# Kernel optimization log

Hardware: AMD Instinct MI355X
Metric: run time of the kernel (lower is better)

Reference implementation:

```python
import jax, jax.numpy as jnp
import numpy as np

H = 128
NUM_IN = 384
B, N, K = 4, 2048, 48
SCALE = 30.0
EPS = 1e-5


def _layernorm(x, gamma, beta):
    mu = jnp.mean(x, axis=-1, keepdims=True)
    var = jnp.mean(jnp.square(x - mu), axis=-1, keepdims=True)
    return (x - mu) * jax.lax.rsqrt(var + EPS) * gamma + beta


def setup_inputs() -> dict:
    key = jax.random.key(0)
    ks = jax.random.split(key, 12)
    s = lambda fan_in: 1.0 / np.sqrt(fan_in)
    inp = {
        "h_V": jax.random.normal(ks[0], (B, N, H), jnp.float32),
        "h_E": jax.random.normal(ks[1], (B, N, K, NUM_IN), jnp.float32),
        "mask_V": jnp.ones((B, N), jnp.float32),
        "mask_attend": jnp.ones((B, N, K), jnp.float32),
        # message MLP
        "W1": jax.random.uniform(ks[2], (H + NUM_IN, H), jnp.float32, -s(H + NUM_IN), s(H + NUM_IN)),
        "b1": jnp.zeros((H,), jnp.float32),
        "W2": jax.random.uniform(ks[3], (H, H), jnp.float32, -s(H), s(H)),
        "b2": jnp.zeros((H,), jnp.float32),
        "W3": jax.random.uniform(ks[4], (H, H), jnp.float32, -s(H), s(H)),
        "b3": jnp.zeros((H,), jnp.float32),
        # layernorms
        "g1": jnp.ones((H,), jnp.float32), "be1": jnp.zeros((H,), jnp.float32),
        "g2": jnp.ones((H,), jnp.float32), "be2": jnp.zeros((H,), jnp.float32),
        # FFN
        "Wi": jax.random.uniform(ks[5], (H, 4 * H), jnp.float32, -s(H), s(H)),
        "bi": jnp.zeros((4 * H,), jnp.float32),
        "Wo": jax.random.uniform(ks[6], (4 * H, H), jnp.float32, -s(4 * H), s(4 * H)),
        "bo": jnp.zeros((H,), jnp.float32),
        # rezero alpha (init 0.01)
        "alpha": jnp.array([0.01], jnp.float32),
    }
    return inp


def reference(h_V, h_E, mask_V, mask_attend, W1, b1, W2, b2, W3, b3,
              g1, be1, g2, be2, Wi, bi, Wo, bo, alpha):
    gelu = lambda x: jax.nn.gelu(x, approximate=False)
    # broadcast-concat node features onto each neighbor edge: [B,N,K,H+num_in]
    h_V_expand = jnp.broadcast_to(h_V[:, :, None, :], (*h_E.shape[:-1], h_V.shape[-1]))
    h_EV = jnp.concatenate([h_V_expand, h_E], axis=-1)
    # 3-layer message MLP
    h_message = gelu(jnp.einsum("bnkf,fh->bnkh", h_EV, W1) + b1)
    h_message = gelu(jnp.einsum("bnkh,hg->bnkg", h_message, W2) + b2)
    h_message = jnp.einsum("bnkg,gh->bnkh", h_message, W3) + b3
    h_message = mask_attend[..., None] * h_message
    # masked sum-reduce over neighbors
    dh = jnp.sum(h_message, axis=-2) / SCALE
    # residual (rezero) + LayerNorm  (dropout = identity in eval)
    h = _layernorm(alpha * dh + h_V, g1, be1)
    # position-wise FFN
    dh = gelu(h @ Wi + bi) @ Wo + bo
    h = _layernorm(alpha * dh + h, g2, be2)
    # node mask
    h = mask_V[..., None] * h
    return h
```

## Files before the change

kernel.cpp:

```cpp
#include <hip/hip_runtime.h>

#define LN_EPS 1e-5f
#define RSCALE (1.0f / 30.0f)

typedef short short8  __attribute__((ext_vector_type(8)));
typedef short short4v __attribute__((ext_vector_type(4)));
typedef float f32x4   __attribute__((ext_vector_type(4)));

__device__ __forceinline__ unsigned short f2bf(float f) {
    unsigned u = __builtin_bit_cast(unsigned, f);
    u = u + 0x7FFFu + ((u >> 16) & 1u);
    return (unsigned short)(u >> 16);
}

__device__ __forceinline__ float gelu_f(float x) {
    float u  = 0.7978845608028654f * (x + 0.044715f * x * x * x);
    float e  = __expf(-2.0f * fabsf(u));
    float t  = 1.0f - 2.0f * e / (1.0f + e);
    return 0.5f * x * (1.0f + copysignf(t, u));
}

__device__ __forceinline__ f32x4 zero4() {
    f32x4 v; v.x = 0.f; v.y = 0.f; v.z = 0.f; v.w = 0.f; return v;
}

__global__ __launch_bounds__(256) void prep_w(
    const float* __restrict__ W1, const float* __restrict__ W2,
    const float* __restrict__ W3,
    unsigned short* __restrict__ w1t, unsigned short* __restrict__ w2t,
    unsigned short* __restrict__ w3t)
{
    int t = blockIdx.x * 256 + threadIdx.x;
    if (t < 65536) {
        int m = t & 127, k = t >> 7;
        w1t[m * 512 + k] = f2bf(W1[k * 128 + m]);
    } else if (t < 81920) {
        int u = t - 65536, m = u & 127, k = u >> 7;
        w2t[m * 128 + k] = f2bf(W2[k * 128 + m]);
    } else if (t < 98304) {
        int u = t - 81920, m = u & 127, k = u >> 7;
        w3t[m * 128 + k] = f2bf(W3[k * 128 + m]);
    }
}

__global__ __launch_bounds__(256, 2) void edge_mlp(
    const float* __restrict__ hV, const float* __restrict__ hE,
    const float* __restrict__ mAtt,
    const unsigned short* __restrict__ w1t, const unsigned short* __restrict__ w2t,
    const unsigned short* __restrict__ w3t,
    const float* __restrict__ b1, const float* __restrict__ b2,
    const float* __restrict__ b3, float* __restrict__ dh)
{
    __shared__ short A1[96 * 64];
    __shared__ short Wb[128 * 64];
    __shared__ short Hb[2][96 * 128];
    __shared__ float mb[96];

    const int tid  = threadIdx.x;
    const int lane = tid & 63;
    const int wv   = tid >> 6;
    const int g    = wv & 1;
    const int mh   = wv >> 1;
    const int ln   = lane & 15;
    const int kg   = lane >> 4;
    const int node0 = blockIdx.x * 2;

    if (tid < 96) mb[tid] = mAtt[node0 * 48 + tid];

    f32x4 acc[4][3];
#pragma unroll
    for (int j = 0; j < 4; ++j)
#pragma unroll
        for (int i = 0; i < 3; ++i) acc[j][i] = zero4();

    const int srow = tid >> 4;
    const int c4   = (tid & 15) * 4;
    const int kb_w = c4 >> 3;
    const int c4lo = c4 & 4;

    for (int c = 0; c < 8; ++c) {
        const int kc = c * 64;
        if (kc < 128) {
#pragma unroll
            for (int rep = 0; rep < 6; ++rep) {
                const int r = rep * 16 + srow;
                const float4 v = *(const float4*)(hV + (node0 + (r >= 48 ? 1 : 0)) * 128 + kc + c4);
                short4v p;
                p.x = (short)f2bf(v.x); p.y = (short)f2bf(v.y);
                p.z = (short)f2bf(v.z); p.w = (short)f2bf(v.w);
                *(short4v*)&A1[r * 64 + ((kb_w ^ (r & 7)) * 8) + c4lo] = p;
            }
        } else {
#pragma unroll
            for (int rep = 0; rep < 6; ++rep) {
                const int r = rep * 16 + srow;
                const float4 v = *(const float4*)(hE + (node0 * 48 + r) * 384 + (kc - 128) + c4);
                short4v p;
                p.x = (short)f2bf(v.x); p.y = (short)f2bf(v.y);
                p.z = (short)f2bf(v.z); p.w = (short)f2bf(v.w);
                *(short4v*)&A1[r * 64 + ((kb_w ^ (r & 7)) * 8) + c4lo] = p;
            }
        }
#pragma unroll
        for (int rep = 0; rep < 4; ++rep) {
            const int u = rep * 256 + tid;
            const int m = u >> 3, kb = u & 7;
            short8 val = *(const short8*)(w1t + m * 512 + kc + kb * 8);
            *(short8*)&Wb[m * 64 + ((kb ^ (m & 7)) * 8)] = val;
        }
        __syncthreads();
#pragma unroll
        for (int s = 0; s < 2; ++s) {
            const int kb = s * 4 + kg;
            short8 bf[3], af[4];
#pragma unroll
            for (int i = 0; i < 3; ++i) {
                const int r = (3 * g + i) * 16 + ln;
                bf[i] = *(const short8*)&A1[r * 64 + ((kb ^ (r & 7)) * 8)];
            }
#pragma unroll
            for (int j = 0; j < 4; ++j) {
                const int m = (4 * mh + j) * 16 + ln;
                af[j] = *(const short8*)&Wb[m * 64 + ((kb ^ (m & 7)) * 8)];
            }
#pragma unroll
            for (int j = 0; j < 4; ++j)
#pragma unroll
                for (int i = 0; i < 3; ++i)
                    acc[j][i] = __builtin_amdgcn_mfma_f32_16x16x32_bf16(af[j], bf[i], acc[j][i], 0, 0, 0);
        }
        __syncthreads();
    }

#pragma unroll
    for (int j = 0; j < 4; ++j) {
        const int m0 = (4 * mh + j) * 16 + kg * 4;
        const float4 bb = *(const float4*)(b1 + m0);
#pragma unroll
        for (int i = 0; i < 3; ++i) {
            const int r = (3 * g + i) * 16 + ln;
            short4v p;
            p.x = (short)f2bf(gelu_f(acc[j][i].x + bb.x));
            p.y = (short)f2bf(gelu_f(acc[j][i].y + bb.y));
            p.z = (short)f2bf(gelu_f(acc[j][i].z + bb.z));
            p.w = (short)f2bf(gelu_f(acc[j][i].w + bb.w));
            *(short4v*)&Hb[0][r * 128 + (((m0 >> 3) ^ (r & 7)) * 8) + (m0 & 4)] = p;
        }
    }

    for (int L = 0; L < 2; ++L) {
#pragma unroll
        for (int j = 0; j < 4; ++j)
#pragma unroll
            for (int i = 0; i < 3; ++i) acc[j][i] = zero4();

        const unsigned short* wt = (L == 0) ? w2t : w3t;
        for (int c = 0; c < 2; ++c) {
            const int kc = c * 64;
#pragma unroll
            for (int rep = 0; rep < 4; ++rep) {
                const int u = rep * 256 + tid;
                const int m = u >> 3, kb = u & 7;
                short8 val = *(const short8*)(wt + m * 128 + kc + kb * 8);
                *(short8*)&Wb[m * 64 + ((kb ^ (m & 7)) * 8)] = val;
            }
            __syncthreads();
#pragma unroll
            for (int s = 0; s < 2; ++s) {
                const int kbW = s * 4 + kg;
                const int kbH = c * 8 + s * 4 + kg;
                short8 bf[3], af[4];
#pragma unroll
                for (int i = 0; i < 3; ++i) {
                    const int r = (3 * g + i) * 16 + ln;
                    bf[i] = *(const short8*)&Hb[L][r * 128 + ((kbH ^ (r & 7)) * 8)];
                }
#pragma unroll
                for (int j = 0; j < 4; ++j) {
                    const int m = (4 * mh + j) * 16 + ln;
                    af[j] = *(const short8*)&Wb[m * 64 + ((kbW ^ (m & 7)) * 8)];
                }
#pragma unroll
                for (int j = 0; j < 4; ++j)
#pragma unroll
                    for (int i = 0; i < 3; ++i)
                        acc[j][i] = __builtin_amdgcn_mfma_f32_16x16x32_bf16(af[j], bf[i], acc[j][i], 0, 0, 0);
            }
            __syncthreads();
        }

        if (L == 0) {
#pragma unroll
            for (int j = 0; j < 4; ++j) {
                const int m0 = (4 * mh + j) * 16 + kg * 4;
                const float4 bb = *(const float4*)(b2 + m0);
#pragma unroll
                for (int i = 0; i < 3; ++i) {
                    const int r = (3 * g + i) * 16 + ln;
                    short4v p;
                    p.x = (short)f2bf(gelu_f(acc[j][i].x + bb.x));
                    p.y = (short)f2bf(gelu_f(acc[j][i].y + bb.y));
                    p.z = (short)f2bf(gelu_f(acc[j][i].z + bb.z));
                    p.w = (short)f2bf(gelu_f(acc[j][i].w + bb.w));
                    *(short4v*)&Hb[1][r * 128 + (((m0 >> 3) ^ (r & 7)) * 8) + (m0 & 4)] = p;
                }
            }
        } else {
#pragma unroll
            for (int j = 0; j < 4; ++j) {
                const int m0 = (4 * mh + j) * 16 + kg * 4;
                const float4 bb = *(const float4*)(b3 + m0);
                float s0 = 0.f, s1 = 0.f, s2 = 0.f, s3 = 0.f;
#pragma unroll
                for (int i = 0; i < 3; ++i) {
                    const int r = (3 * g + i) * 16 + ln;
                    const float mk = mb[r];
                    s0 += (acc[j][i].x + bb.x) * mk;
                    s1 += (acc[j][i].y + bb.y) * mk;
                    s2 += (acc[j][i].z + bb.z) * mk;
                    s3 += (acc[j][i].w + bb.w) * mk;
                }
#pragma unroll
                for (int off = 1; off < 16; off <<= 1) {
                    s0 += __shfl_xor(s0, off, 64);
                    s1 += __shfl_xor(s1, off, 64);
                    s2 += __shfl_xor(s2, off, 64);
                    s3 += __shfl_xor(s3, off, 64);
                }
                if (ln == 0) {
                    float4 o;
                    o.x = s0 * RSCALE; o.y = s1 * RSCALE;
                    o.z = s2 * RSCALE; o.w = s3 * RSCALE;
                    *(float4*)&dh[(node0 + g) * 128 + m0] = o;
                }
            }
        }
    }
}

__global__ __launch_bounds__(256, 2) void node_ffn(
    const float* __restrict__ hV, const float* __restrict__ dh,
    const float* __restrict__ maskV,
    const float* __restrict__ g1, const float* __restrict__ be1,
    const float* __restrict__ g2, const float* __restrict__ be2,
    const float* __restrict__ Wi, const float* __restrict__ bi,
    const float* __restrict__ Wo, const float* __restrict__ bo,
    const float* __restrict__ alphap, float* __restrict__ out)
{
    __shared__ float hbuf[16 * 132];
    __shared__ float hidb[16 * 516];
    __shared__ float obuf[16 * 132];

    const int tid = threadIdx.x;
    const float al = alphap[0];
    const int nb = blockIdx.x * 16;

    {
        const int m = tid >> 4, s = tid & 15;
        const int i0 = s * 8;
        const int base = (nb + m) * 128 + i0;
        float x[8];
        {
            float4 a0 = *(const float4*)(dh + base);
            float4 a1 = *(const float4*)(dh + base + 4);
            float4 v0 = *(const float4*)(hV + base);
            float4 v1 = *(const float4*)(hV + base + 4);
            x[0] = v0.x + al * a0.x; x[1] = v0.y + al * a0.y;
            x[2] = v0.z + al * a0.z; x[3] = v0.w + al * a0.w;
            x[4] = v1.x + al * a1.x; x[5] = v1.y + al * a1.y;
            x[6] = v1.z + al * a1.z; x[7] = v1.w + al * a1.w;
        }
        float sm = 0.f;
#pragma unroll
        for (int q = 0; q < 8; ++q) sm += x[q];
#pragma unroll
        for (int off = 1; off < 16; off <<= 1) sm += __shfl_xor(sm, off, 64);
        const float mu = sm * (1.0f / 128.0f);
        float vs = 0.f;
#pragma unroll
        for (int q = 0; q < 8; ++q) { float d = x[q] - mu; vs += d * d; }
#pragma unroll
        for (int off = 1; off < 16; off <<= 1) vs += __shfl_xor(vs, off, 64);
        const float rs = rsqrtf(vs * (1.0f / 128.0f) + LN_EPS);
#pragma unroll
        for (int q = 0; q < 8; ++q)
            hbuf[m * 132 + i0 + q] = (x[q] - mu) * rs * g1[i0 + q] + be1[i0 + q];
    }
    __syncthreads();

    {
        const int jg = tid & 127, mhh = tid >> 7;
        const int j4 = jg * 4;
        float acc[8][4];
#pragma unroll
        for (int mm = 0; mm < 8; ++mm)
#pragma unroll
            for (int jj = 0; jj < 4; ++jj) acc[mm][jj] = 0.f;
        for (int i0 = 0; i0 < 128; i0 += 4) {
            float4 w0 = *(const float4*)(Wi + (i0 + 0) * 512 + j4);
            float4 w1 = *(const float4*)(Wi + (i0 + 1) * 512 + j4);
            float4 w2 = *(const float4*)(Wi + (i0 + 2) * 512 + j4);
            float4 w3 = *(const float4*)(Wi + (i0 + 3) * 512 + j4);
#pragma unroll
            for (int mm = 0; mm < 8; ++mm) {
                float4 h4 = *(const float4*)&hbuf[(mhh * 8 + mm) * 132 + i0];
                acc[mm][0] += h4.x * w0.x + h4.y * w1.x + h4.z * w2.x + h4.w * w3.x;
                acc[mm][1] += h4.x * w0.y + h4.y * w1.y + h4.z * w2.y + h4.w * w3.y;
                acc[mm][2] += h4.x * w0.z + h4.y * w1.z + h4.z * w2.z + h4.w * w3.z;
                acc[mm][3] += h4.x * w0.w + h4.y * w1.w + h4.z * w2.w + h4.w * w3.w;
            }
        }
        float4 bb = *(const float4*)(bi + j4);
#pragma unroll
        for (int mm = 0; mm < 8; ++mm) {
            float4 o;
            o.x = gelu_f(acc[mm][0] + bb.x);
            o.y = gelu_f(acc[mm][1] + bb.y);
            o.z = gelu_f(acc[mm][2] + bb.z);
            o.w = gelu_f(acc[mm][3] + bb.w);
            *(float4*)&hidb[(mhh * 8 + mm) * 516 + j4] = o;
        }
    }
    __syncthreads();

    {
        const int m = tid >> 4;
        const int n8 = (tid & 15) * 8;
        float4 r0, r1;
        r0.x = r0.y = r0.z = r0.w = 0.f;
        r1.x = r1.y = r1.z = r1.w = 0.f;
        for (int j0 = 0; j0 < 512; j0 += 4) {
            float4 hh = *(const float4*)&hidb[m * 516 + j0];
            float hq[4] = {hh.x, hh.y, hh.z, hh.w};
#pragma unroll
            for (int jj = 0; jj < 4; ++jj) {
                float4 w0 = *(const float4*)(Wo + (j0 + jj) * 128 + n8);
                float4 w1 = *(const float4*)(Wo + (j0 + jj) * 128 + n8 + 4);
                r0.x += hq[jj] * w0.x; r0.y += hq[jj] * w0.y;
                r0.z += hq[jj] * w0.z; r0.w += hq[jj] * w0.w;
                r1.x += hq[jj] * w1.x; r1.y += hq[jj] * w1.y;
                r1.z += hq[jj] * w1.z; r1.w += hq[jj] * w1.w;
            }
        }
        float4 q0 = *(const float4*)(bo + n8);
        float4 q1 = *(const float4*)(bo + n8 + 4);
        r0.x += q0.x; r0.y += q0.y; r0.z += q0.z; r0.w += q0.w;
        r1.x += q1.x; r1.y += q1.y; r1.z += q1.z; r1.w += q1.w;
        *(float4*)&obuf[m * 132 + n8]     = r0;
        *(float4*)&obuf[m * 132 + n8 + 4] = r1;
    }
    __syncthreads();

    {
        const int m = tid >> 4, s = tid & 15;
        const int i0 = s * 8;
        float x[8];
#pragma unroll
        for (int q = 0; q < 8; ++q)
            x[q] = hbuf[m * 132 + i0 + q] + al * obuf[m * 132 + i0 + q];
        float sm = 0.f;
#pragma unroll
        for (int q = 0; q < 8; ++q) sm += x[q];
#pragma unroll
        for (int off = 1; off < 16; off <<= 1) sm += __shfl_xor(sm, off, 64);
        const float mu = sm * (1.0f / 128.0f);
        float vs = 0.f;
#pragma unroll
        for (int q = 0; q < 8; ++q) { float d = x[q] - mu; vs += d * d; }
#pragma unroll
        for (int off = 1; off < 16; off <<= 1) vs += __shfl_xor(vs, off, 64);
        const float rs = rsqrtf(vs * (1.0f / 128.0f) + LN_EPS);
        const float mk = maskV[nb + m];
        float y[8];
#pragma unroll
        for (int q = 0; q < 8; ++q)
            y[q] = ((x[q] - mu) * rs * g2[i0 + q] + be2[i0 + q]) * mk;
        float4 o0, o1;
        o0.x = y[0]; o0.y = y[1]; o0.z = y[2]; o0.w = y[3];
        o1.x = y[4]; o1.y = y[5]; o1.z = y[6]; o1.w = y[7];
        const int base = (nb + m) * 128 + i0;
        *(float4*)(out + base)     = o0;
        *(float4*)(out + base + 4) = o1;
    }
}

extern "C" void kernel_launch(void* const* d_in, const int* in_sizes, int n_in,
                              void* d_out, int out_size, void* d_ws, size_t ws_size,
                              hipStream_t stream)
{
    const float* hV  = (const float*)d_in[0];
    const float* hE  = (const float*)d_in[1];
    const float* mV  = (const float*)d_in[2];
    const float* mA  = (const float*)d_in[3];
    const float* W1  = (const float*)d_in[4];
    const float* b1  = (const float*)d_in[5];
    const float* W2  = (const float*)d_in[6];
    const float* b2  = (const float*)d_in[7];
    const float* W3  = (const float*)d_in[8];
    const float* b3  = (const float*)d_in[9];
    const float* g1  = (const float*)d_in[10];
    const float* be1 = (const float*)d_in[11];
    const float* g2  = (const float*)d_in[12];
    const float* be2 = (const float*)d_in[13];
    const float* Wi  = (const float*)d_in[14];
    const float* bi  = (const float*)d_in[15];
    const float* Wo  = (const float*)d_in[16];
    const float* bo  = (const float*)d_in[17];
    const float* al  = (const float*)d_in[18];
    float* out = (float*)d_out;

    float* dh = (float*)d_ws;
    unsigned short* w1t = (unsigned short*)((char*)d_ws + (size_t)4194304);
    unsigned short* w2t = w1t + 65536;
    unsigned short* w3t = w2t + 16384;

    prep_w  <<<384,  256, 0, stream>>>(W1, W2, W3, w1t, w2t, w3t);
    edge_mlp<<<4096, 256, 0, stream>>>(hV, hE, mA, w1t, w2t, w3t, b1, b2, b3, dh);
    node_ffn<<<512,  256, 0, stream>>>(hV, dh, mV, g1, be1, g2, be2, Wi, bi, Wo, bo, al, out);
}
```

Baseline: 991.8 us.

## Restructure edge MLP to one node per wave with direct global operand loads

Each wave now owns a whole node (48 edges by 128 outputs), so the cross-wave shared staging and all block-level barriers in the edge MLP go away. Weight fragments are read straight from global memory (relying on L1/L2 caching) and h_E rows are loaded into registers with a one-step software prefetch. The h_V part of the first layer is computed once per node and copied into all three edge accumulators instead of being redone for every edge row. The cost is heavier register use (24 accumulators plus prefetch buffers) and repeated global weight reads by every wave, which may lower occupancy.

```diff
diff --git a/kernel.cpp b/kernel.cpp
--- a/kernel.cpp
+++ b/kernel.cpp
@@ -18,6 +18,15 @@
     float e  = __expf(-2.0f * fabsf(u));
     float t  = 1.0f - 2.0f * e / (1.0f + e);
     return 0.5f * x * (1.0f + copysignf(t, u));
+}
+
+__device__ __forceinline__ short8 cvt8(float4 a, float4 b) {
+    short8 r;
+    r[0] = (short)f2bf(a.x); r[1] = (short)f2bf(a.y);
+    r[2] = (short)f2bf(a.z); r[3] = (short)f2bf(a.w);
+    r[4] = (short)f2bf(b.x); r[5] = (short)f2bf(b.y);
+    r[6] = (short)f2bf(b.z); r[7] = (short)f2bf(b.w);
+    return r;
 }
 
 __device__ __forceinline__ f32x4 zero4() {
@@ -51,174 +60,140 @@
     const float* __restrict__ b1, const float* __restrict__ b2,
     const float* __restrict__ b3, float* __restrict__ dh)
 {
-    __shared__ short A1[96 * 64];
-    __shared__ short Wb[128 * 64];
-    __shared__ short Hb[2][96 * 128];
-    __shared__ float mb[96];
+    __shared__ short Hs[4][48 * 128];
 
     const int tid  = threadIdx.x;
+    const int wv   = tid >> 6;
     const int lane = tid & 63;
-    const int wv   = tid >> 6;
-    const int g    = wv & 1;
-    const int mh   = wv >> 1;
     const int ln   = lane & 15;
     const int kg   = lane >> 4;
-    const int node0 = blockIdx.x * 2;
-
-    if (tid < 96) mb[tid] = mAtt[node0 * 48 + tid];
-
-    f32x4 acc[4][3];
-#pragma unroll
-    for (int j = 0; j < 4; ++j)
-#pragma unroll
-        for (int i = 0; i < 3; ++i) acc[j][i] = zero4();
-
-    const int srow = tid >> 4;
-    const int c4   = (tid & 15) * 4;
-    const int kb_w = c4 >> 3;
-    const int c4lo = c4 & 4;
-
-    for (int c = 0; c < 8; ++c) {
-        const int kc = c * 64;
-        if (kc < 128) {
-#pragma unroll
-            for (int rep = 0; rep < 6; ++rep) {
-                const int r = rep * 16 + srow;
-                const float4 v = *(const float4*)(hV + (node0 + (r >= 48 ? 1 : 0)) * 128 + kc + c4);
-                short4v p;
-                p.x = (short)f2bf(v.x); p.y = (short)f2bf(v.y);
-                p.z = (short)f2bf(v.z); p.w = (short)f2bf(v.w);
-                *(short4v*)&A1[r * 64 + ((kb_w ^ (r & 7)) * 8) + c4lo] = p;
-            }
-        } else {
-#pragma unroll
-            for (int rep = 0; rep < 6; ++rep) {
-                const int r = rep * 16 + srow;
-                const float4 v = *(const float4*)(hE + (node0 * 48 + r) * 384 + (kc - 128) + c4);
-                short4v p;
-                p.x = (short)f2bf(v.x); p.y = (short)f2bf(v.y);
-                p.z = (short)f2bf(v.z); p.w = (short)f2bf(v.w);
-                *(short4v*)&A1[r * 64 + ((kb_w ^ (r & 7)) * 8) + c4lo] = p;
-            }
-        }
-#pragma unroll
-        for (int rep = 0; rep < 4; ++rep) {
-            const int u = rep * 256 + tid;
-            const int m = u >> 3, kb = u & 7;
-            short8 val = *(const short8*)(w1t + m * 512 + kc + kb * 8);
-            *(short8*)&Wb[m * 64 + ((kb ^ (m & 7)) * 8)] = val;
-        }
-        __syncthreads();
-#pragma unroll
-        for (int s = 0; s < 2; ++s) {
-            const int kb = s * 4 + kg;
-            short8 bf[3], af[4];
+    const int node = blockIdx.x * 4 + wv;
+    short* Hw = &Hs[wv][0];
+
+    f32x4 acc[8][3];
+
+#pragma unroll
+    for (int j = 0; j < 8; ++j) acc[j][0] = zero4();
+#pragma unroll
+    for (int ks = 0; ks < 4; ++ks) {
+        const float* hp = hV + node * 128 + ks * 32 + kg * 8;
+        float4 v0 = *(const float4*)hp;
+        float4 v1 = *(const float4*)(hp + 4);
+        short8 bf = cvt8(v0, v1);
+#pragma unroll
+        for (int j = 0; j < 8; ++j) {
+            short8 af = *(const short8*)(w1t + (j * 16 + ln) * 512 + ks * 32 + kg * 8);
+            acc[j][0] = __builtin_amdgcn_mfma_f32_16x16x32_bf16(af, bf, acc[j][0], 0, 0, 0);
+        }
+    }
+#pragma unroll
+    for (int j = 0; j < 8; ++j) { acc[j][1] = acc[j][0]; acc[j][2] = acc[j][0]; }
+
+    float4 e0[3], e1[3];
+#pragma unroll
+    for (int i = 0; i < 3; ++i) {
+        const float* p = hE + (node * 48 + 16 * i + ln) * 384 + kg * 8;
+        e0[i] = *(const float4*)p;
+        e1[i] = *(const float4*)(p + 4);
+    }
+    for (int ks = 4; ks < 16; ++ks) {
+        float4 f0[3], f1[3];
+        if (ks < 15) {
 #pragma unroll
             for (int i = 0; i < 3; ++i) {
-                const int r = (3 * g + i) * 16 + ln;
-                bf[i] = *(const short8*)&A1[r * 64 + ((kb ^ (r & 7)) * 8)];
-            }
-#pragma unroll
-            for (int j = 0; j < 4; ++j) {
-                const int m = (4 * mh + j) * 16 + ln;
-                af[j] = *(const short8*)&Wb[m * 64 + ((kb ^ (m & 7)) * 8)];
-            }
-#pragma unroll
-            for (int j = 0; j < 4; ++j)
-#pragma unroll
-                for (int i = 0; i < 3; ++i)
-                    acc[j][i] = __builtin_amdgcn_mfma_f32_16x16x32_bf16(af[j], bf[i], acc[j][i], 0, 0, 0);
-        }
-        __syncthreads();
-    }
-
-#pragma unroll
-    for (int j = 0; j < 4; ++j) {
-        const int m0 = (4 * mh + j) * 16 + kg * 4;
-        const float4 bb = *(const float4*)(b1 + m0);
+                const float* p = hE + (node * 48 + 16 * i + ln) * 384 + (ks - 3) * 32 + kg * 8;
+                f0[i] = *(const float4*)p;
+                f1[i] = *(const float4*)(p + 4);
+            }
+        }
+        short8 bf[3];
+#pragma unroll
+        for (int i = 0; i < 3; ++i) bf[i] = cvt8(e0[i], e1[i]);
+#pragma unroll
+        for (int j = 0; j < 8; ++j) {
+            short8 af = *(const short8*)(w1t + (j * 16 + ln) * 512 + ks * 32 + kg * 8);
+#pragma unroll
+            for (int i = 0; i < 3; ++i)
+                acc[j][i] = __builtin_amdgcn_mfma_f32_16x16x32_bf16(af, bf[i], acc[j][i], 0, 0, 0);
+        }
+#pragma unroll
+        for (int i = 0; i < 3; ++i) { e0[i] = f0[i]; e1[i] = f1[i]; }
+    }
+
+#pragma unroll
+    for (int j = 0; j < 8; ++j) {
+        const float4 bb = *(const float4*)(b1 + j * 16 + 4 * kg);
+        const int blk0 = 2 * j + (kg >> 1);
+        const int off  = 4 * (kg & 1);
 #pragma unroll
         for (int i = 0; i < 3; ++i) {
-            const int r = (3 * g + i) * 16 + ln;
+            const int n = 16 * i + ln;
             short4v p;
             p.x = (short)f2bf(gelu_f(acc[j][i].x + bb.x));
             p.y = (short)f2bf(gelu_f(acc[j][i].y + bb.y));
             p.z = (short)f2bf(gelu_f(acc[j][i].z + bb.z));
             p.w = (short)f2bf(gelu_f(acc[j][i].w + bb.w));
-            *(short4v*)&Hb[0][r * 128 + (((m0 >> 3) ^ (r & 7)) * 8) + (m0 & 4)] = p;
+            *(short4v*)&Hw[n * 128 + ((blk0 ^ (n & 7)) * 8) + off] = p;
         }
     }
 
     for (int L = 0; L < 2; ++L) {
-#pragma unroll
-        for (int j = 0; j < 4; ++j)
-#pragma unroll
-            for (int i = 0; i < 3; ++i) acc[j][i] = zero4();
-
         const unsigned short* wt = (L == 0) ? w2t : w3t;
-        for (int c = 0; c < 2; ++c) {
-            const int kc = c * 64;
-#pragma unroll
-            for (int rep = 0; rep < 4; ++rep) {
-                const int u = rep * 256 + tid;
-                const int m = u >> 3, kb = u & 7;
-                short8 val = *(const short8*)(wt + m * 128 + kc + kb * 8);
-                *(short8*)&Wb[m * 64 + ((kb ^ (m & 7)) * 8)] = val;
-            }
-            __syncthreads();
-#pragma unroll
-            for (int s = 0; s < 2; ++s) {
-                const int kbW = s * 4 + kg;
-                const int kbH = c * 8 + s * 4 + kg;
-                short8 bf[3], af[4];
+        f32x4 a2[8][3];
+#pragma unroll
+        for (int j = 0; j < 8; ++j)
+#pragma unroll
+            for (int i = 0; i < 3; ++i) a2[j][i] = zero4();
+
+#pragma unroll
+        for (int c = 0; c < 4; ++c) {
+            short8 hb[3];
+#pragma unroll
+            for (int i = 0; i < 3; ++i) {
+                const int n = 16 * i + ln;
+                const int blk = (c * 4 + kg) ^ (n & 7);
+                hb[i] = *(const short8*)&Hw[n * 128 + blk * 8];
+            }
+#pragma unroll
+            for (int j = 0; j < 8; ++j) {
+                short8 af = *(const short8*)(wt + (j * 16 + ln) * 128 + c * 32 + kg * 8);
+#pragma unroll
+                for (int i = 0; i < 3; ++i)
+                    a2[j][i] = __builtin_amdgcn_mfma_f32_16x16x32_bf16(af, hb[i], a2[j][i], 0, 0, 0);
+            }
+        }
+
+        if (L == 0) {
+#pragma unroll
+            for (int j = 0; j < 8; ++j) {
+                const float4 bb = *(const float4*)(b2 + j * 16 + 4 * kg);
+                const int blk0 = 2 * j + (kg >> 1);
+                const int off  = 4 * (kg & 1);
 #pragma unroll
                 for (int i = 0; i < 3; ++i) {
-                    const int r = (3 * g + i) * 16 + ln;
-                    bf[i] = *(const short8*)&Hb[L][r * 128 + ((kbH ^ (r & 7)) * 8)];
+                    const int n = 16 * i + ln;
+                    short4v p;
+                    p.x = (short)f2bf(gelu_f(a2[j][i].x + bb.x));
+                    p.y = (short)f2bf(gelu_f(a2[j][i].y + bb.y));
+                    p.z = (short)f2bf(gelu_f(a2[j][i].z + bb.z));
+                    p.w = (short)f2bf(gelu_f(a2[j][i].w + bb.w));
+                    *(short4v*)&Hw[n * 128 + ((blk0 ^ (n & 7)) * 8) + off] = p;
                 }
-#pragma unroll
-                for (int j = 0; j < 4; ++j) {
-                    const int m = (4 * mh + j) * 16 + ln;
-                    af[j] = *(const short8*)&Wb[m * 64 + ((kbW ^ (m & 7)) * 8)];
-                }
-#pragma unroll
-                for (int j = 0; j < 4; ++j)
-#pragma unroll
-                    for (int i = 0; i < 3; ++i)
-                        acc[j][i] = __builtin_amdgcn_mfma_f32_16x16x32_bf16(af[j], bf[i], acc[j][i], 0, 0, 0);
-            }
-            __syncthreads();
-        }
-
-        if (L == 0) {
-#pragma unroll
-            for (int j = 0; j < 4; ++j) {
-                const int m0 = (4 * mh + j) * 16 + kg * 4;
-                const float4 bb = *(const float4*)(b2 + m0);
+            }
+        } else {
+            float mk[3];
+#pragma unroll
+            for (int i = 0; i < 3; ++i) mk[i] = mAtt[node * 48 + 16 * i + ln];
+#pragma unroll
+            for (int j = 0; j < 8; ++j) {
+                const float4 bb = *(const float4*)(b3 + j * 16 + 4 * kg);
+                float s0 = 0.f, s1 = 0.f, s2 = 0.f, s3 = 0.f;
 #pragma unroll
                 for (int i = 0; i < 3; ++i) {
-                    const int r = (3 * g + i) * 16 + ln;
-                    short4v p;
-                    p.x = (short)f2bf(gelu_f(acc[j][i].x + bb.x));
-                    p.y = (short)f2bf(gelu_f(acc[j][i].y + bb.y));
-                    p.z = (short)f2bf(gelu_f(acc[j][i].z + bb.z));
-                    p.w = (short)f2bf(gelu_f(acc[j][i].w + bb.w));
-                    *(short4v*)&Hb[1][r * 128 + (((m0 >> 3) ^ (r & 7)) * 8) + (m0 & 4)] = p;
-                }
-            }
-        } else {
-#pragma unroll
-            for (int j = 0; j < 4; ++j) {
-                const int m0 = (4 * mh + j) * 16 + kg * 4;
-                const float4 bb = *(const float4*)(b3 + m0);
-                float s0 = 0.f, s1 = 0.f, s2 = 0.f, s3 = 0.f;
-#pragma unroll
-                for (int i = 0; i < 3; ++i) {
-                    const int r = (3 * g + i) * 16 + ln;
-                    const float mk = mb[r];
-                    s0 += (acc[j][i].x + bb.x) * mk;
-                    s1 += (acc[j][i].y + bb.y) * mk;
-                    s2 += (acc[j][i].z + bb.z) * mk;
-                    s3 += (acc[j][i].w + bb.w) * mk;
+                    s0 += (a2[j][i].x + bb.x) * mk[i];
+                    s1 += (a2[j][i].y + bb.y) * mk[i];
+                    s2 += (a2[j][i].z + bb.z) * mk[i];
+                    s3 += (a2[j][i].w + bb.w) * mk[i];
                 }
 #pragma unroll
                 for (int off = 1; off < 16; off <<= 1) {
@@ -231,7 +206,7 @@
                     float4 o;
                     o.x = s0 * RSCALE; o.y = s1 * RSCALE;
                     o.z = s2 * RSCALE; o.w = s3 * RSCALE;
-                    *(float4*)&dh[(node0 + g) * 128 + m0] = o;
+                    *(float4*)&dh[node * 128 + j * 16 + 4 * kg] = o;
                 }
             }
         }
@@ -415,6 +390,6 @@
     unsigned short* w3t = w2t + 16384;
 
     prep_w  <<<384,  256, 0, stream>>>(W1, W2, W3, w1t, w2t, w3t);
-    edge_mlp<<<4096, 256, 0, stream>>>(hV, hE, mA, w1t, w2t, w3t, b1, b2, b3, dh);
+    edge_mlp<<<2048, 256, 0, stream>>>(hV, hE, mA, w1t, w2t, w3t, b1, b2, b3, dh);
     node_ffn<<<512,  256, 0, stream>>>(hV, dh, mV, g1, be1, g2, be2, Wi, bi, Wo, bo, al, out);
 }
```

Result: slower. 1.066 ms (+7.5%).
